# Optimization experiments

Hardware: AMD Instinct MI355X
Metric: run time of the kernel (lower is better)

The kernel has to match this reference:

```python
import jax, jax.numpy as jnp
import numpy as np

B, C, H = 16, 512, 32
HID, NB, S, P, SR = 512, 36, 26, 7, 2
SCALE = 32.0
N_LOC, N_LOC_LAB = 12, 8
N_GRP, GRP_SZ, N_GRP_LAB = 4, 6, 16
IN_DIM = P * P * C


def roi_align(feat, coords, scale, pooled, sr):
    # feat: (B,C,H,W); coords: (B,NB,4) normalized xyxy. torchvision roi_align,
    # aligned=False, fixed sampling_ratio=sr (adaptive ratio is data-dependent).
    Bs, Cc, Hh, Ww = feat.shape
    x1 = coords[..., 0] * scale
    y1 = coords[..., 1] * scale
    x2 = coords[..., 2] * scale
    y2 = coords[..., 3] * scale
    rw = jnp.maximum(x2 - x1, 1.0)
    rh = jnp.maximum(y2 - y1, 1.0)
    bw = rw / pooled
    bh = rh / pooled
    # sample offsets within roi, in bin units: (pooled*sr,)
    off = (jnp.arange(pooled)[:, None] + (jnp.arange(sr) + 0.5) / sr).reshape(-1)
    ys = y1[..., None] + off * bh[..., None]  # (B,NB,pooled*sr)
    xs = x1[..., None] + off * bw[..., None]

    def prep(t, size):
        valid = (t > -1.0) & (t < size)
        tc = jnp.clip(t, 0.0, size - 1)
        lo = jnp.floor(tc).astype(jnp.int32)
        hi = jnp.minimum(lo + 1, size - 1)
        frac = tc - lo
        return lo, hi, frac, valid

    y_lo, y_hi, ly, vy = prep(ys, Hh)
    x_lo, x_hi, lx, vx = prep(xs, Ww)
    hy, hx = 1.0 - ly, 1.0 - lx

    featl = feat.transpose(0, 2, 3, 1)  # (B,H,W,C)
    b_idx = jnp.arange(Bs)[:, None, None, None]

    def gather(yi, xi):
        # -> (B,NB,Py,Px,C)
        return featl[b_idx, yi[:, :, :, None], xi[:, :, None, :]]

    def w(a, b):
        return (a[..., :, None] * b[..., None, :])[..., None]

    val = (gather(y_lo, x_lo) * w(hy, hx) + gather(y_lo, x_hi) * w(hy, lx)
           + gather(y_hi, x_lo) * w(ly, hx) + gather(y_hi, x_hi) * w(ly, lx))
    mask = (vy[:, :, :, None] & vx[:, :, None, :])[..., None]
    val = jnp.where(mask, val, 0.0)
    val = val.reshape(Bs, -1, pooled, sr, pooled, sr, Cc).mean(axis=(3, 5))
    return val.transpose(0, 1, 4, 2, 3)  # (B,NB,C,pooled,pooled)


def setup_inputs() -> dict:
    key = jax.random.key(0)
    ks = jax.random.split(key, 10)
    lf = jax.random.normal(ks[0], (B, C, H, H), dtype=jnp.float32)
    xs = jnp.sort(jax.random.uniform(ks[1], (B, S, 2)), axis=-1)
    ys = jnp.sort(jax.random.uniform(ks[2], (B, S, 2)), axis=-1)
    coords = jnp.stack([xs[..., 0], ys[..., 0], xs[..., 1], ys[..., 1]], axis=-1)
    sc = 0.02
    return {
        'local_features': lf,
        'pred_bbox_coords': coords,
        'roi_fc_W': jax.random.normal(ks[3], (HID, IN_DIM), dtype=jnp.float32) * sc,
        'roi_fc_b': jnp.zeros((HID,), jnp.float32),
        'coords_W': jax.random.normal(ks[4], (S, 4, HID), dtype=jnp.float32) * sc,
        'coords_b': jnp.zeros((S, 4), jnp.float32),
        'pres_W': jax.random.normal(ks[5], (S, HID), dtype=jnp.float32) * sc,
        'pres_b': jnp.zeros((S,), jnp.float32),
        'loc_W': jax.random.normal(ks[6], (N_LOC, N_LOC_LAB, HID), dtype=jnp.float32) * sc,
        'loc_b': jnp.zeros((N_LOC, N_LOC_LAB), jnp.float32),
        'grp_W': jax.random.normal(ks[7], (N_GRP, N_GRP_LAB, GRP_SZ * HID), dtype=jnp.float32) * sc,
        'grp_b': jnp.zeros((N_GRP, N_GRP_LAB), jnp.float32),
        'loc_idx': jnp.arange(N_LOC, dtype=jnp.int32),
        'grp_idx': jnp.arange(N_GRP * GRP_SZ, dtype=jnp.int32).reshape(N_GRP, GRP_SZ),
    }


def reference(local_features, pred_bbox_coords, roi_fc_W, roi_fc_b, coords_W,
              coords_b, pres_W, pres_b, loc_W, loc_b, grp_W, grp_b, loc_idx, grp_idx):
    Bs = local_features.shape[0]
    # boxes S..NB default to the full image (0,0,1,1)
    full = jnp.broadcast_to(jnp.array([0.0, 0.0, 1.0, 1.0], jnp.float32), (Bs, NB, 4))
    coords_all = full.at[:, :S].set(pred_bbox_coords)
    roi = roi_align(local_features, coords_all, SCALE, P, SR)  # (B,NB,C,P,P)
    flat = roi.reshape(Bs, NB, IN_DIM)
    feats = jax.nn.relu(jnp.einsum('bnf,hf->bnh', flat, roi_fc_W) + roi_fc_b)
    sup = feats[:, :S]  # (B,S,HID)
    # per-box coord refinement heads
    deltas = jnp.einsum('bsh,soh->bso', sup, coords_W) + coords_b  # (B,S,4)
    w = pred_bbox_coords[..., 2] - pred_bbox_coords[..., 0]
    h = pred_bbox_coords[..., 3] - pred_bbox_coords[..., 1]
    wh = jnp.stack([w, h, w, h], axis=-1)
    refined = pred_bbox_coords + deltas * wh
    presence = jnp.einsum('bsh,sh->bs', sup, pres_W) + pres_b  # (B,S)
    # per-box MLC heads
    loc = jnp.einsum('blh,loh->blo', feats[:, loc_idx], loc_W) + loc_b
    # per-group MLC heads (concat box feats within group along hidden)
    gf = feats[:, grp_idx].reshape(Bs, N_GRP, GRP_SZ * HID)
    grp = jnp.einsum('bgk,gok->bgo', gf, grp_W) + grp_b
    mlc = jnp.concatenate([loc.reshape(Bs, -1), grp.reshape(Bs, -1)], axis=1)
    return refined, presence, mlc
```

## Files before the change

kernel.cpp:

```cpp
#include <hip/hip_runtime.h>

typedef unsigned short u16;
typedef __attribute__((ext_vector_type(8))) short short8;
typedef __attribute__((ext_vector_type(8))) unsigned short ushort8_t;
typedef __attribute__((ext_vector_type(4))) float f32x4;
typedef __attribute__((ext_vector_type(2))) float v2f;

#define BATCH   16
#define CCH     512
#define NBOX    36
#define SS      26
#define INDIM   25088
#define HIDN    512
#define M_ROWS  576
#define KSPLIT  28
#define KITERS  14

__device__ __forceinline__ u16 f2bf(float f) {
  unsigned u = __float_as_uint(f);
  u += 0x7FFF + ((u >> 16) & 1);
  return (u16)(u >> 16);
}
__device__ __forceinline__ float bf2f(u16 h) {
  return __uint_as_float(((unsigned)h) << 16);
}
__device__ __forceinline__ v2f bf2x2(u16 a, u16 b) {
  v2f r;
  r.x = __uint_as_float(((unsigned)a) << 16);
  r.y = __uint_as_float(((unsigned)b) << 16);
  return r;
}

__global__ __launch_bounds__(256) void k_transpose_lf(const float* __restrict__ in,
                                                      u16* __restrict__ out) {
  __shared__ u16 t[32][66];
  int b = blockIdx.z, y = blockIdx.y, ct = blockIdx.x;
  int tid = threadIdx.x;

  int cl = tid >> 2;
  int xq = (tid & 3) * 8;
  const float* src = in + ((size_t)(b * CCH + ct * 64 + cl) * 1024) + y * 32 + xq;
  float4 v0 = *(const float4*)src;
  float4 v1 = *(const float4*)(src + 4);
  t[xq + 0][cl] = f2bf(v0.x); t[xq + 1][cl] = f2bf(v0.y);
  t[xq + 2][cl] = f2bf(v0.z); t[xq + 3][cl] = f2bf(v0.w);
  t[xq + 4][cl] = f2bf(v1.x); t[xq + 5][cl] = f2bf(v1.y);
  t[xq + 6][cl] = f2bf(v1.z); t[xq + 7][cl] = f2bf(v1.w);
  __syncthreads();

  int xl = tid >> 3;
  int cq = (tid & 7) * 8;
  ushort8_t o;
#pragma unroll
  for (int i = 0; i < 8; ++i) o[i] = t[xl][cq + i];
  *(ushort8_t*)(out + ((size_t)b * 1024 + y * 32 + xl) * CCH + ct * 64 + cq) = o;
}

__global__ __launch_bounds__(256) void k_convert_w(const float4* __restrict__ in,
                                                   ushort4* __restrict__ out) {
  int i = blockIdx.x * 256 + threadIdx.x;
  float4 v = in[i];
  ushort4 o;
  o.x = f2bf(v.x); o.y = f2bf(v.y); o.z = f2bf(v.z); o.w = f2bf(v.w);
  out[i] = o;
}

__global__ __launch_bounds__(512) void k_roi(const u16* __restrict__ lf_t,
                                             const float* __restrict__ pred,
                                             u16* __restrict__ flat) {
  __shared__ int   s_ylo[14], s_yhi[14], s_xlo[14], s_xhi[14];
  __shared__ float s_wyl[14], s_wyh[14], s_wxl[14], s_wxh[14];
  __shared__ u16   s_out[INDIM];

  int blk = blockIdx.x;
  int b = blk / NBOX, n = blk % NBOX;
  int t = threadIdx.x;

  if (t < 28) {
    bool isY = t < 14;
    int j = isY ? t : t - 14;
    float c0, c1, c2, c3;
    if (n < SS) {
      const float* p = pred + ((size_t)(b * SS + n)) * 4;
      c0 = p[0]; c1 = p[1]; c2 = p[2]; c3 = p[3];
    } else { c0 = 0.f; c1 = 0.f; c2 = 1.f; c3 = 1.f; }
    float lo1 = (isY ? c1 : c0) * 32.f;
    float hi1 = (isY ? c3 : c2) * 32.f;
    float sz = fmaxf(hi1 - lo1, 1.f);
    float bs = sz * (1.f / 7.f);
    float off = (float)(j >> 1) + 0.25f + 0.5f * (float)(j & 1);
    float pos = lo1 + off * bs;
    bool valid = (pos > -1.f) && (pos < 32.f);
    float tc = fminf(fmaxf(pos, 0.f), 31.f);
    int lo = (int)floorf(tc);
    int hi = min(lo + 1, 31);
    float fr = tc - (float)lo;
    float wl = valid ? (1.f - fr) : 0.f;
    float wh = valid ? fr : 0.f;
    if (isY) { s_ylo[j] = lo; s_yhi[j] = hi; s_wyl[j] = wl; s_wyh[j] = wh; }
    else     { s_xlo[j] = lo; s_xhi[j] = hi; s_wxl[j] = wl; s_wxh[j] = wh; }
  }
  __syncthreads();

  int cg = t & 63;
  int pg = t >> 6;
  const u16* base = lf_t + (size_t)b * 1024 * CCH + cg * 8;

  for (int p = pg; p < 49; p += 8) {
    int py = p / 7, px = p % 7;
    v2f a0 = {0.f, 0.f}, a1 = {0.f, 0.f}, a2 = {0.f, 0.f}, a3 = {0.f, 0.f};
#pragma unroll
    for (int sy = 0; sy < 2; ++sy) {
      int jy = 2 * py + sy;
      const u16* rlo = base + s_ylo[jy] * 32 * CCH;
      const u16* rhi = base + s_yhi[jy] * 32 * CCH;
      float wyl = s_wyl[jy], wyh = s_wyh[jy];
#pragma unroll
      for (int sx = 0; sx < 2; ++sx) {
        int jx = 2 * px + sx;
        int xl = s_xlo[jx] * CCH, xh = s_xhi[jx] * CCH;
        v2f wll = {wyl * s_wxl[jx], wyl * s_wxl[jx]};
        v2f wlh = {wyl * s_wxh[jx], wyl * s_wxh[jx]};
        v2f whl = {wyh * s_wxl[jx], wyh * s_wxl[jx]};
        v2f whh = {wyh * s_wxh[jx], wyh * s_wxh[jx]};
        ushort8_t vll = *(const ushort8_t*)(rlo + xl);
        ushort8_t vlh = *(const ushort8_t*)(rlo + xh);
        ushort8_t vhl = *(const ushort8_t*)(rhi + xl);
        ushort8_t vhh = *(const ushort8_t*)(rhi + xh);
        a0 += wll * bf2x2(vll[0], vll[1]) + wlh * bf2x2(vlh[0], vlh[1])
            + whl * bf2x2(vhl[0], vhl[1]) + whh * bf2x2(vhh[0], vhh[1]);
        a1 += wll * bf2x2(vll[2], vll[3]) + wlh * bf2x2(vlh[2], vlh[3])
            + whl * bf2x2(vhl[2], vhl[3]) + whh * bf2x2(vhh[2], vhh[3]);
        a2 += wll * bf2x2(vll[4], vll[5]) + wlh * bf2x2(vlh[4], vlh[5])
            + whl * bf2x2(vhl[4], vhl[5]) + whh * bf2x2(vhh[4], vhh[5]);
        a3 += wll * bf2x2(vll[6], vll[7]) + wlh * bf2x2(vlh[6], vlh[7])
            + whl * bf2x2(vhl[6], vhl[7]) + whh * bf2x2(vhh[6], vhh[7]);
      }
    }
    int c0i = cg * 8;
    s_out[(c0i + 0) * 49 + p] = f2bf(a0.x * 0.25f);
    s_out[(c0i + 1) * 49 + p] = f2bf(a0.y * 0.25f);
    s_out[(c0i + 2) * 49 + p] = f2bf(a1.x * 0.25f);
    s_out[(c0i + 3) * 49 + p] = f2bf(a1.y * 0.25f);
    s_out[(c0i + 4) * 49 + p] = f2bf(a2.x * 0.25f);
    s_out[(c0i + 5) * 49 + p] = f2bf(a2.y * 0.25f);
    s_out[(c0i + 6) * 49 + p] = f2bf(a3.x * 0.25f);
    s_out[(c0i + 7) * 49 + p] = f2bf(a3.y * 0.25f);
  }
  __syncthreads();

  uint4* dst = (uint4*)(flat + (size_t)blk * INDIM);
  const uint4* src = (const uint4*)s_out;
  for (int i = t; i < INDIM / 8; i += 512) dst[i] = src[i];
}

__global__ __launch_bounds__(256) void k_gemm(const u16* __restrict__ flat,
                                              const u16* __restrict__ Wb,
                                              float* __restrict__ partials) {
  __shared__ u16 As[128 * 64];
  __shared__ u16 Bs[128 * 64];

  int tid = threadIdx.x;
  int wave = tid >> 6, lane = tid & 63;
  int wm = wave >> 1, wn = wave & 1;
  int quad = lane >> 4, r = lane & 15;
  int xb = r & 7;

  int tileM0 = blockIdx.y * 128;
  int tileN0 = blockIdx.x * 128;
  int kbase = blockIdx.z * (KITERS * 64);

  size_t aoff[4], boff[4];
  int    ldso[4];
#pragma unroll
  for (int t = 0; t < 4; ++t) {
    int chunk = (wave * 4 + t) * 64 + lane;
    int row = chunk >> 3;
    int lc = chunk & 7;
    ldso[t] = row * 64 + ((lc ^ (row & 7)) << 3);
    int grow = min(tileM0 + row, M_ROWS - 1);
    aoff[t] = (size_t)grow * INDIM + kbase + lc * 8;
    boff[t] = (size_t)(tileN0 + row) * INDIM + kbase + lc * 8;
  }

  f32x4 acc[4][4];
#pragma unroll
  for (int mi = 0; mi < 4; ++mi)
#pragma unroll
    for (int ni = 0; ni < 4; ++ni) acc[mi][ni] = (f32x4){0.f, 0.f, 0.f, 0.f};

  short8 ra[4], rb[4];
#pragma unroll
  for (int t = 0; t < 4; ++t) {
    ra[t] = *(const short8*)(flat + aoff[t]);
    rb[t] = *(const short8*)(Wb + boff[t]);
  }

  for (int kt = 0; kt < KITERS; ++kt) {
#pragma unroll
    for (int t = 0; t < 4; ++t) {
      *(short8*)&As[ldso[t]] = ra[t];
      *(short8*)&Bs[ldso[t]] = rb[t];
    }
    __syncthreads();

    if (kt + 1 < KITERS) {
      int kadv = (kt + 1) * 64;
#pragma unroll
      for (int t = 0; t < 4; ++t) {
        ra[t] = *(const short8*)(flat + aoff[t] + kadv);
        rb[t] = *(const short8*)(Wb + boff[t] + kadv);
      }
    }

#pragma unroll
    for (int kk = 0; kk < 64; kk += 32) {
      int k8 = kk >> 3;
      int pc = ((k8 + quad) ^ xb) << 3;
      short8 af[4], bfr[4];
#pragma unroll
      for (int mi = 0; mi < 4; ++mi)
        af[mi] = *(const short8*)&As[(wm * 64 + mi * 16 + r) * 64 + pc];
#pragma unroll
      for (int ni = 0; ni < 4; ++ni)
        bfr[ni] = *(const short8*)&Bs[(wn * 64 + ni * 16 + r) * 64 + pc];
#pragma unroll
      for (int mi = 0; mi < 4; ++mi)
#pragma unroll
        for (int ni = 0; ni < 4; ++ni)
          acc[mi][ni] = __builtin_amdgcn_mfma_f32_16x16x32_bf16(
              af[mi], bfr[ni], acc[mi][ni], 0, 0, 0);
    }
    __syncthreads();
  }

  float* part = partials + (size_t)blockIdx.z * (M_ROWS * HIDN);
#pragma unroll
  for (int mi = 0; mi < 4; ++mi)
#pragma unroll
    for (int ni = 0; ni < 4; ++ni) {
      int row0 = tileM0 + wm * 64 + mi * 16 + quad * 4;
      int col = tileN0 + wn * 64 + ni * 16 + r;
#pragma unroll
      for (int reg = 0; reg < 4; ++reg) {
        int row = row0 + reg;
        if (row < M_ROWS) part[(size_t)row * HIDN + col] = acc[mi][ni][reg];
      }
    }
}

__global__ __launch_bounds__(256) void k_reduce(const float4* __restrict__ partials,
                                                const float* __restrict__ bias,
                                                float4* __restrict__ feats) {
  int gid = blockIdx.x * 256 + threadIdx.x;
  int h4 = gid & (HIDN / 4 - 1);
  float4 s = {0.f, 0.f, 0.f, 0.f};
#pragma unroll
  for (int k = 0; k < KSPLIT; ++k) {
    float4 v = partials[(size_t)k * (M_ROWS * HIDN / 4) + gid];
    s.x += v.x; s.y += v.y; s.z += v.z; s.w += v.w;
  }
  const float* bi = bias + h4 * 4;
  s.x = fmaxf(s.x + bi[0], 0.f);
  s.y = fmaxf(s.y + bi[1], 0.f);
  s.z = fmaxf(s.z + bi[2], 0.f);
  s.w = fmaxf(s.w + bi[3], 0.f);
  feats[gid] = s;
}

__device__ __forceinline__ float wave_red(float s) {
#pragma unroll
  for (int off = 32; off > 0; off >>= 1) s += __shfl_down(s, off);
  return s;
}

__device__ __forceinline__ float dot512(const float* __restrict__ f,
                                        const float* __restrict__ w, int lane) {
  const float4* f4 = (const float4*)f;
  const float4* w4 = (const float4*)w;
  float4 x0 = f4[lane], y0 = w4[lane];
  float4 x1 = f4[lane + 64], y1 = w4[lane + 64];
  return x0.x * y0.x + x0.y * y0.y + x0.z * y0.z + x0.w * y0.w +
         x1.x * y1.x + x1.y * y1.y + x1.z * y1.z + x1.w * y1.w;
}

__global__ __launch_bounds__(256) void k_heads(const float* __restrict__ feats,
                                               const float* __restrict__ pred,
                                               const float* __restrict__ cW,
                                               const float* __restrict__ cb,
                                               const float* __restrict__ pW,
                                               const float* __restrict__ pb,
                                               const float* __restrict__ lW,
                                               const float* __restrict__ lb,
                                               const float* __restrict__ gW,
                                               const float* __restrict__ gb,
                                               const int* __restrict__ lidx,
                                               const int* __restrict__ gidx,
                                               float* __restrict__ out) {
  int wid = blockIdx.x * 4 + (threadIdx.x >> 6);
  int lane = threadIdx.x & 63;
  float sum = 0.f;

  if (wid < 1664) {
    int b = wid / 104, rr = wid % 104, s = rr >> 2, o = rr & 3;
    sum = dot512(feats + (size_t)(b * NBOX + s) * HIDN,
                 cW + (size_t)(s * 4 + o) * HIDN, lane);
    sum = wave_red(sum);
    if (lane == 0) {
      const float* p = pred + (size_t)(b * SS + s) * 4;
      float wdt = p[2] - p[0], hgt = p[3] - p[1];
      float whv = (o & 1) ? hgt : wdt;
      out[wid] = p[o] + (sum + cb[s * 4 + o]) * whv;
    }
  } else if (wid < 2080) {
    int i = wid - 1664;
    int b = i / 26, s = i % 26;
    sum = dot512(feats + (size_t)(b * NBOX + s) * HIDN,
                 pW + (size_t)s * HIDN, lane);
    sum = wave_red(sum);
    if (lane == 0) out[1664 + i] = sum + pb[s];
  } else if (wid < 3616) {
    int i = wid - 2080;
    int b = i / 96, rr = i % 96, l = rr >> 3, o = rr & 7;
    sum = dot512(feats + (size_t)(b * NBOX + lidx[l]) * HIDN,
                 lW + (size_t)(l * 8 + o) * HIDN, lane);
    sum = wave_red(sum);
    if (lane == 0) out[2080 + b * 160 + rr] = sum + lb[l * 8 + o];
  } else {
    int i = wid - 3616;
    int b = i / 64, rr = i % 64, g = rr >> 4, o = rr & 15;
    const float* w = gW + (size_t)(g * 16 + o) * 3072;
#pragma unroll
    for (int jj = 0; jj < 6; ++jj) {
      sum += dot512(feats + (size_t)(b * NBOX + gidx[g * 6 + jj]) * HIDN,
                    w + jj * 512, lane);
    }
    sum = wave_red(sum);
    if (lane == 0) out[2080 + b * 160 + 96 + rr] = sum + gb[g * 16 + o];
  }
}

extern "C" void kernel_launch(void* const* d_in, const int* in_sizes, int n_in,
                              void* d_out, int out_size, void* d_ws, size_t ws_size,
                              hipStream_t stream) {
  const float* lf      = (const float*)d_in[0];
  const float* pred    = (const float*)d_in[1];
  const float* roiW    = (const float*)d_in[2];
  const float* roiB    = (const float*)d_in[3];
  const float* cW      = (const float*)d_in[4];
  const float* cb      = (const float*)d_in[5];
  const float* pW      = (const float*)d_in[6];
  const float* pb      = (const float*)d_in[7];
  const float* lW      = (const float*)d_in[8];
  const float* lb      = (const float*)d_in[9];
  const float* gW      = (const float*)d_in[10];
  const float* gb      = (const float*)d_in[11];
  const int*   lidx    = (const int*)d_in[12];
  const int*   gidx    = (const int*)d_in[13];
  float* out = (float*)d_out;

  char* ws = (char*)d_ws;
  u16*   lf_t     = (u16*)ws;
  float* partials = (float*)ws;
  u16*   Wb   = (u16*)(ws + 33030144);
  u16*   flat = (u16*)(ws + 33030144 + 25690112);
  float* feats = (float*)(ws + 33030144 + 25690112 + 28901376);

  k_transpose_lf<<<dim3(8, 32, 16), 256, 0, stream>>>(lf, lf_t);
  k_convert_w<<<12544, 256, 0, stream>>>((const float4*)roiW, (ushort4*)Wb);
  k_roi<<<576, 512, 0, stream>>>(lf_t, pred, flat);
  k_gemm<<<dim3(4, 5, KSPLIT), 256, 0, stream>>>(flat, Wb, partials);
  k_reduce<<<(M_ROWS * HIDN / 4) / 256, 256, 0, stream>>>(
      (const float4*)partials, roiB, (float4*)feats);
  k_heads<<<1160, 256, 0, stream>>>(feats, pred, cW, cb, pW, pb, lW, lb, gW, gb,
                                    lidx, gidx, out);
}
```

Measured before the change: 221.0 us.

## Reorder GEMM operands into k-block-major tiles, drop ROI shared-memory staging

The ROI kernel now writes each thread's 8 channels straight to global memory in a k-block-major layout (K ordered as pixel then channel), so the shared staging buffer and the copy-out pass go away. The weight conversion kernel permutes the roi_fc weights the same way, using per-row shared-memory staging, so both GEMM operands share the new K order. The GEMM then reads contiguous 64-wide k-blocks for each k-step instead of rows strided by INDIM. This cuts shared-memory use and a sync in the ROI kernel and should improve load locality in the GEMM. The cost is a heavier weight-conversion kernel: 512 blocks each using about 52 KB of shared memory, with a divide by 49 per element.

```diff
diff --git a/kernel.cpp b/kernel.cpp
--- a/kernel.cpp
+++ b/kernel.cpp
@@ -15,6 +15,7 @@
 #define M_ROWS  576
 #define KSPLIT  28
 #define KITERS  14
+#define NKB     392
 
 __device__ __forceinline__ u16 f2bf(float f) {
   unsigned u = __float_as_uint(f);
@@ -56,21 +57,43 @@
   *(ushort8_t*)(out + ((size_t)b * 1024 + y * 32 + xl) * CCH + ct * 64 + cq) = o;
 }
 
-__global__ __launch_bounds__(256) void k_convert_w(const float4* __restrict__ in,
-                                                   ushort4* __restrict__ out) {
-  int i = blockIdx.x * 256 + threadIdx.x;
-  float4 v = in[i];
-  ushort4 o;
-  o.x = f2bf(v.x); o.y = f2bf(v.y); o.z = f2bf(v.z); o.w = f2bf(v.w);
-  out[i] = o;
+#define WPAD 532
+__global__ __launch_bounds__(256) void k_convert_w(const float* __restrict__ in,
+                                                   u16* __restrict__ out) {
+  __shared__ u16 s[49 * WPAD];
+  int h = blockIdx.x;
+  int tid = threadIdx.x;
+  const float4* src = (const float4*)(in + (size_t)h * INDIM);
+  for (int i = tid; i < 6272; i += 256) {
+    float4 v = src[i];
+    int k = i * 4;
+#pragma unroll
+    for (int j = 0; j < 4; ++j) {
+      int kk = k + j;
+      int c = kk / 49;
+      int p = kk - c * 49;
+      s[p * WPAD + c] = f2bf((&v.x)[j]);
+    }
+  }
+  __syncthreads();
+  for (int q = tid; q < 3136; q += 256) {
+    int p = q >> 6;
+    int c0 = (q & 63) * 8;
+    const u16* sp = &s[p * WPAD + c0];
+    ushort8_t o;
+#pragma unroll
+    for (int i = 0; i < 8; ++i) o[i] = sp[i];
+    int kb = p * 8 + (c0 >> 6);
+    int col = c0 & 63;
+    *(ushort8_t*)(out + ((size_t)kb * HIDN + h) * 64 + col) = o;
+  }
 }
 
 __global__ __launch_bounds__(512) void k_roi(const u16* __restrict__ lf_t,
                                              const float* __restrict__ pred,
-                                             u16* __restrict__ flat) {
+                                             u16* __restrict__ flat2) {
   __shared__ int   s_ylo[14], s_yhi[14], s_xlo[14], s_xhi[14];
   __shared__ float s_wyl[14], s_wyh[14], s_wxl[14], s_wxh[14];
-  __shared__ u16   s_out[INDIM];
 
   int blk = blockIdx.x;
   int b = blk / NBOX, n = blk % NBOX;
@@ -137,25 +160,19 @@
             + whl * bf2x2(vhl[6], vhl[7]) + whh * bf2x2(vhh[6], vhh[7]);
       }
     }
-    int c0i = cg * 8;
-    s_out[(c0i + 0) * 49 + p] = f2bf(a0.x * 0.25f);
-    s_out[(c0i + 1) * 49 + p] = f2bf(a0.y * 0.25f);
-    s_out[(c0i + 2) * 49 + p] = f2bf(a1.x * 0.25f);
-    s_out[(c0i + 3) * 49 + p] = f2bf(a1.y * 0.25f);
-    s_out[(c0i + 4) * 49 + p] = f2bf(a2.x * 0.25f);
-    s_out[(c0i + 5) * 49 + p] = f2bf(a2.y * 0.25f);
-    s_out[(c0i + 6) * 49 + p] = f2bf(a3.x * 0.25f);
-    s_out[(c0i + 7) * 49 + p] = f2bf(a3.y * 0.25f);
-  }
-  __syncthreads();
-
-  uint4* dst = (uint4*)(flat + (size_t)blk * INDIM);
-  const uint4* src = (const uint4*)s_out;
-  for (int i = t; i < INDIM / 8; i += 512) dst[i] = src[i];
-}
-
-__global__ __launch_bounds__(256) void k_gemm(const u16* __restrict__ flat,
-                                              const u16* __restrict__ Wb,
+    ushort8_t o;
+    o[0] = f2bf(a0.x * 0.25f); o[1] = f2bf(a0.y * 0.25f);
+    o[2] = f2bf(a1.x * 0.25f); o[3] = f2bf(a1.y * 0.25f);
+    o[4] = f2bf(a2.x * 0.25f); o[5] = f2bf(a2.y * 0.25f);
+    o[6] = f2bf(a3.x * 0.25f); o[7] = f2bf(a3.y * 0.25f);
+    int kb = p * 8 + (cg >> 3);
+    int col = (cg & 7) * 8;
+    *(ushort8_t*)(flat2 + ((size_t)kb * M_ROWS + blk) * 64 + col) = o;
+  }
+}
+
+__global__ __launch_bounds__(256) void k_gemm(const u16* __restrict__ flat2,
+                                              const u16* __restrict__ Wb2,
                                               float* __restrict__ partials) {
   __shared__ u16 As[128 * 64];
   __shared__ u16 Bs[128 * 64];
@@ -168,7 +185,7 @@
 
   int tileM0 = blockIdx.y * 128;
   int tileN0 = blockIdx.x * 128;
-  int kbase = blockIdx.z * (KITERS * 64);
+  int kb0 = blockIdx.z * KITERS;
 
   size_t aoff[4], boff[4];
   int    ldso[4];
@@ -179,8 +196,8 @@
     int lc = chunk & 7;
     ldso[t] = row * 64 + ((lc ^ (row & 7)) << 3);
     int grow = min(tileM0 + row, M_ROWS - 1);
-    aoff[t] = (size_t)grow * INDIM + kbase + lc * 8;
-    boff[t] = (size_t)(tileN0 + row) * INDIM + kbase + lc * 8;
+    aoff[t] = ((size_t)kb0 * M_ROWS + grow) * 64 + lc * 8;
+    boff[t] = ((size_t)kb0 * HIDN + tileN0 + row) * 64 + lc * 8;
   }
 
   f32x4 acc[4][4];
@@ -192,8 +209,8 @@
   short8 ra[4], rb[4];
 #pragma unroll
   for (int t = 0; t < 4; ++t) {
-    ra[t] = *(const short8*)(flat + aoff[t]);
-    rb[t] = *(const short8*)(Wb + boff[t]);
+    ra[t] = *(const short8*)(flat2 + aoff[t]);
+    rb[t] = *(const short8*)(Wb2 + boff[t]);
   }
 
   for (int kt = 0; kt < KITERS; ++kt) {
@@ -205,11 +222,12 @@
     __syncthreads();
 
     if (kt + 1 < KITERS) {
-      int kadv = (kt + 1) * 64;
+      size_t ak = (size_t)(kt + 1) * (M_ROWS * 64);
+      size_t bk = (size_t)(kt + 1) * (HIDN * 64);
 #pragma unroll
       for (int t = 0; t < 4; ++t) {
-        ra[t] = *(const short8*)(flat + aoff[t] + kadv);
-        rb[t] = *(const short8*)(Wb + boff[t] + kadv);
+        ra[t] = *(const short8*)(flat2 + aoff[t] + ak);
+        rb[t] = *(const short8*)(Wb2 + boff[t] + bk);
       }
     }
 
@@ -362,14 +380,14 @@
   char* ws = (char*)d_ws;
   u16*   lf_t     = (u16*)ws;
   float* partials = (float*)ws;
-  u16*   Wb   = (u16*)(ws + 33030144);
-  u16*   flat = (u16*)(ws + 33030144 + 25690112);
+  u16*   Wb2   = (u16*)(ws + 33030144);
+  u16*   flat2 = (u16*)(ws + 33030144 + 25690112);
   float* feats = (float*)(ws + 33030144 + 25690112 + 28901376);
 
   k_transpose_lf<<<dim3(8, 32, 16), 256, 0, stream>>>(lf, lf_t);
-  k_convert_w<<<12544, 256, 0, stream>>>((const float4*)roiW, (ushort4*)Wb);
-  k_roi<<<576, 512, 0, stream>>>(lf_t, pred, flat);
-  k_gemm<<<dim3(4, 5, KSPLIT), 256, 0, stream>>>(flat, Wb, partials);
+  k_convert_w<<<HIDN, 256, 0, stream>>>(roiW, Wb2);
+  k_roi<<<576, 512, 0, stream>>>(lf_t, pred, flat2);
+  k_gemm<<<dim3(4, 5, KSPLIT), 256, 0, stream>>>(flat2, Wb2, partials);
   k_reduce<<<(M_ROWS * HIDN / 4) / 256, 256, 0, stream>>>(
       (const float4*)partials, roiB, (float4*)feats);
   k_heads<<<1160, 256, 0, stream>>>(feats, pred, cW, cb, pW, pb, lW, lb, gW, gb,
```

Result: slower. 231.9 us (+4.9%).
